# Kernel optimization log

Hardware: AMD Instinct MI355X
Metric: run time of the kernel (lower is better)

Reference implementation:

```python
import jax, jax.numpy as jnp
import numpy as np


def _gelu(x):
    return jax.nn.gelu(x, approximate=False)


def _conv2d(x, w, b, pad=0, dil=1, groups=1):
    y = jax.lax.conv_general_dilated(
        x, w, (1, 1), [(pad, pad), (pad, pad)], rhs_dilation=(dil, dil),
        dimension_numbers=('NCHW', 'OIHW', 'NCHW'), feature_group_count=groups)
    return y + b[None, :, None, None]


def _ln_last(x, g, b, eps=1e-5):
    m = jnp.mean(x, -1, keepdims=True)
    v = jnp.var(x, -1, keepdims=True)
    return (x - m) * jax.lax.rsqrt(v + eps) * g + b


def _ln2d(x, g, b, eps=1e-5):
    # LayerNorm over channel dim of NCHW
    m = jnp.mean(x, 1, keepdims=True)
    v = jnp.var(x, 1, keepdims=True)
    return (x - m) * jax.lax.rsqrt(v + eps) * g[None, :, None, None] + b[None, :, None, None]


def _bilinear(x, py, px):
    # x: [B,C,H,W]; py,px: [B,H,W] float sample coords; zero outside
    B, C, H, W = x.shape
    y0 = jnp.floor(py)
    x0 = jnp.floor(px)
    wy = py - y0
    wx = px - x0
    xf = x.reshape(B, C, H * W)

    def g(yi, xi):
        valid = ((yi >= 0) & (yi < H) & (xi >= 0) & (xi < W)).astype(x.dtype)
        yc = jnp.clip(yi, 0, H - 1).astype(jnp.int32)
        xc = jnp.clip(xi, 0, W - 1).astype(jnp.int32)
        idx = (yc * W + xc).reshape(B, 1, H * W)
        v = jnp.take_along_axis(xf, idx, axis=2).reshape(B, C, H, W)
        return v * valid[:, None]

    return (g(y0, x0) * ((1 - wy) * (1 - wx))[:, None]
            + g(y0, x0 + 1) * ((1 - wy) * wx)[:, None]
            + g(y0 + 1, x0) * (wy * (1 - wx))[:, None]
            + g(y0 + 1, x0 + 1) * (wy * wx)[:, None])


def _deform_dw(x, ow, ob, w, b, dil):
    # modulated deformable depthwise 3x3 conv, offset_groups=1
    B, C, H, W = x.shape
    pad = dil
    off = _conv2d(x, ow, ob, pad=pad, dil=dil)          # [B,27,H,W]
    ox, oy, m = jnp.split(off, 3, axis=1)               # each [B,9,H,W]
    m = jax.nn.sigmoid(m)
    ys = jnp.arange(H, dtype=x.dtype)[None, :, None]
    xs = jnp.arange(W, dtype=x.dtype)[None, None, :]
    acc = jnp.zeros_like(x)
    for ki in range(3):
        for kj in range(3):
            kk = ki * 3 + kj
            py = ys - pad + ki * dil + oy[:, kk]
            px = xs - pad + kj * dil + ox[:, kk]
            s = _bilinear(x, py, px)                    # [B,C,H,W]
            acc = acc + s * m[:, kk][:, None] * w[:, 0, ki, kj][None, :, None, None]
    return acc + b[None, :, None, None]


def _forward(image_embed, inter_prototypes, intra_prototypes, masks,
             proj_w, proj_b, lin_w, lin_b, tok_g, tok_b, alpha,
             in_w, in_b, off0_w, off0_b, dw0_w, dw0_b,
             off1_w, off1_b, dw1_w, dw1_b, cv_w, cv_b, ln_g, ln_b,
             op0_w, op0_b, op1_w, op1_b, op2_w, op2_b,
             out0_w, out0_b, out1_w, out1_b):
    C = image_embed.shape[1]
    scale = C ** -0.5
    # prototype tokens [B,Q,C]
    pt = jnp.einsum('bqc,bnc->bqn', inter_prototypes, intra_prototypes)
    t = jnp.concatenate([inter_prototypes, pt], axis=-1) @ proj_w + proj_b
    t = _gelu(t) @ lin_w + lin_b
    t = _ln_last(t, tok_g, tok_b)
    # mask gating of image features
    pe = jnp.einsum('bnc,bnhw->bchw', intra_prototypes, masks)
    img = image_embed * pe + image_embed
    # DeformAttn
    x = _gelu(_conv2d(img, in_w, in_b))
    a = _deform_dw(x, off0_w, off0_b, dw0_w, dw0_b, dil=1)
    a = _deform_dw(a, off1_w, off1_b, dw1_w, dw1_b, dil=3)
    a = _conv2d(a, cv_w, cv_b)
    x = x * a + img
    x = _ln2d(x, ln_g, ln_b)
    y = _conv2d(x, op0_w, op0_b)
    y = _gelu(_conv2d(y, op1_w, op1_b, pad=1, groups=C))
    y = _conv2d(y, op2_w, op2_b)
    dense = y + x
    # prototype cross-attention over 8 tokens
    attn = jnp.einsum('bchw,bqc->bqhw', dense, t) * scale
    attn = jax.nn.softmax(attn, axis=1)
    attn = jnp.einsum('bqhw,bqc->bchw', attn, t)
    attn = attn + dense * alpha[None, :, None, None]
    o = _gelu(_conv2d(attn, out0_w, out0_b))
    o = _conv2d(o, out1_w, out1_b)
    return o


def setup_inputs():
    key = jax.random.key(0)
    ks = jax.random.split(key, 40)
    B, C, H, W, Q, N = 16, 256, 64, 64, 8, 9
    f32 = jnp.float32

    def rn(k, shp, s=1.0):
        return jax.random.normal(k, shp, f32) * s

    inp = {
        'image_embed': rn(ks[0], (B, C, H, W)),
        'inter_prototypes': rn(ks[1], (B, Q, C)),
        'intra_prototypes': rn(ks[2], (B, N, C)),
        'masks': jax.random.uniform(ks[3], (B, N, H, W), f32),
        'proj_w': rn(ks[4], (C + N, C), 0.02), 'proj_b': jnp.zeros((C,), f32),
        'lin_w': rn(ks[5], (C, C), 0.02), 'lin_b': jnp.zeros((C,), f32),
        'tok_g': 1.0 + rn(ks[6], (C,), 0.05), 'tok_b': rn(ks[7], (C,), 0.05),
        'alpha': jnp.ones((C,), f32) * 0.001,
        'in_w': rn(ks[8], (C, C, 1, 1), 0.02), 'in_b': jnp.zeros((C,), f32),
        'off0_w': rn(ks[9], (27, C, 3, 3), 0.01), 'off0_b': rn(ks[10], (27,), 0.01),
        'dw0_w': rn(ks[11], (C, 1, 3, 3), 0.2), 'dw0_b': jnp.zeros((C,), f32),
        'off1_w': rn(ks[12], (27, C, 3, 3), 0.01), 'off1_b': rn(ks[13], (27,), 0.01),
        'dw1_w': rn(ks[14], (C, 1, 3, 3), 0.2), 'dw1_b': jnp.zeros((C,), f32),
        'cv_w': rn(ks[15], (C, C, 1, 1), 0.02), 'cv_b': jnp.zeros((C,), f32),
        'ln_g': 1.0 + rn(ks[16], (C,), 0.05), 'ln_b': rn(ks[17], (C,), 0.05),
        'op0_w': rn(ks[18], (C, C, 1, 1), 0.02), 'op0_b': jnp.zeros((C,), f32),
        'op1_w': rn(ks[19], (C, 1, 3, 3), 0.2), 'op1_b': jnp.zeros((C,), f32),
        'op2_w': rn(ks[20], (C, C, 1, 1), 0.02), 'op2_b': jnp.zeros((C,), f32),
        'out0_w': rn(ks[21], (C // 2, C, 1, 1), 0.02), 'out0_b': jnp.zeros((C // 2,), f32),
        'out1_w': rn(ks[22], (C, C // 2, 1, 1), 0.02), 'out1_b': jnp.zeros((C,), f32),
    }
    return inp


def reference(image_embed, inter_prototypes, intra_prototypes, masks,
              proj_w, proj_b, lin_w, lin_b, tok_g, tok_b, alpha,
              in_w, in_b, off0_w, off0_b, dw0_w, dw0_b,
              off1_w, off1_b, dw1_w, dw1_b, cv_w, cv_b, ln_g, ln_b,
              op0_w, op0_b, op1_w, op1_b, op2_w, op2_b,
              out0_w, out0_b, out1_w, out1_b):
    return _forward(image_embed, inter_prototypes, intra_prototypes, masks,
                    proj_w, proj_b, lin_w, lin_b, tok_g, tok_b, alpha,
                    in_w, in_b, off0_w, off0_b, dw0_w, dw0_b,
                    off1_w, off1_b, dw1_w, dw1_b, cv_w, cv_b, ln_g, ln_b,
                    op0_w, op0_b, op1_w, op1_b, op2_w, op2_b,
                    out0_w, out0_b, out1_w, out1_b)
```

## Files before the change

### kernel.cpp

```cpp
#include <hip/hip_runtime.h>
#include <math.h>

#define BB 16
#define CC 256
#define HH 64
#define WW 64
#define HWs 4096
#define PP 65536
#define QQ 8
#define NN 9

typedef _Float16 half8_t __attribute__((ext_vector_type(8)));
typedef _Float16 half4_t __attribute__((ext_vector_type(4)));
typedef _Float16 half2_t __attribute__((ext_vector_type(2)));
typedef float floatx4 __attribute__((ext_vector_type(4)));

__device__ __forceinline__ float gelu_f(float x) {
    return 0.5f * x * (1.0f + erff(x * 0.70710678118654752f));
}

__global__ void prep_weights_kernel(const float* __restrict__ off0_w, const float* __restrict__ off1_w,
                                    const float* __restrict__ dw0_w, const float* __restrict__ dw1_w,
                                    const float* __restrict__ op1_w,
                                    const float* __restrict__ in_w, const float* __restrict__ cv_w,
                                    const float* __restrict__ op0_w, const float* __restrict__ op2_w,
                                    const float* __restrict__ out0_w, const float* __restrict__ out1_w,
                                    float* __restrict__ dwt0, float* __restrict__ dwt1,
                                    float* __restrict__ op1t,
                                    _Float16* __restrict__ wh_in, _Float16* __restrict__ wh_cv,
                                    _Float16* __restrict__ wh_op0, _Float16* __restrict__ wh_op2,
                                    _Float16* __restrict__ wh_out0, _Float16* __restrict__ wh_out1,
                                    _Float16* __restrict__ whoff0, _Float16* __restrict__ whoff1) {
    int i = blockIdx.x * 256 + threadIdx.x;
    if (i < 9*256) {
        int c = i & 255;
        int tap = i >> 8;
        dwt0[i] = dw0_w[c*9 + tap];
        dwt1[i] = dw1_w[c*9 + tap];
        op1t[i] = op1_w[c*9 + tap];
    }
    if (i < 65536) {
        wh_in[i]  = (_Float16)in_w[i];
        wh_cv[i]  = (_Float16)cv_w[i];
        wh_op0[i] = (_Float16)op0_w[i];
        wh_op2[i] = (_Float16)op2_w[i];
    }
    if (i < 32768) {
        wh_out0[i] = (_Float16)out0_w[i];
        wh_out1[i] = (_Float16)out1_w[i];
    }
    if (i < 9*32*256) {
        int ci = i & 255;
        int k32 = (i >> 8) & 31;
        int tap = i >> 13;
        float v0 = 0.f, v1 = 0.f;
        if (k32 < 27) {
            v0 = off0_w[(k32*256 + ci)*9 + tap];
            v1 = off1_w[(k32*256 + ci)*9 + tap];
        }
        whoff0[i] = (_Float16)v0;
        whoff1[i] = (_Float16)v1;
    }
}

__global__ void token_kernel(const float* __restrict__ inter, const float* __restrict__ intra,
                             const float* __restrict__ proj_w, const float* __restrict__ proj_b,
                             const float* __restrict__ lin_w, const float* __restrict__ lin_b,
                             const float* __restrict__ tok_g, const float* __restrict__ tok_b,
                             float* __restrict__ t_out) {
    int bq = blockIdx.x;
    int b = bq >> 3, q = bq & 7;
    int c = threadIdx.x;
    __shared__ float inter_s[256];
    __shared__ float pt_s[9];
    __shared__ float g_s[256];
    __shared__ float red[256];
    __shared__ float stat[2];
    inter_s[c] = inter[(b*QQ + q)*CC + c];
    __syncthreads();
    for (int n = 0; n < 9; n++) {
        red[c] = inter_s[c] * intra[(b*NN + n)*CC + c];
        __syncthreads();
        for (int s = 128; s > 0; s >>= 1) {
            if (c < s) red[c] += red[c + s];
            __syncthreads();
        }
        if (c == 0) pt_s[n] = red[0];
        __syncthreads();
    }
    float u = proj_b[c];
    for (int k = 0; k < 256; k++) u += inter_s[k] * proj_w[k*CC + c];
    for (int n = 0; n < 9; n++) u += pt_s[n] * proj_w[(256 + n)*CC + c];
    g_s[c] = gelu_f(u);
    __syncthreads();
    float v = lin_b[c];
    for (int k = 0; k < 256; k++) v += g_s[k] * lin_w[k*CC + c];
    red[c] = v;
    __syncthreads();
    for (int s = 128; s > 0; s >>= 1) { if (c < s) red[c] += red[c + s]; __syncthreads(); }
    if (c == 0) stat[0] = red[0] * (1.0f/256.0f);
    __syncthreads();
    float m = stat[0];
    red[c] = (v - m)*(v - m);
    __syncthreads();
    for (int s = 128; s > 0; s >>= 1) { if (c < s) red[c] += red[c + s]; __syncthreads(); }
    if (c == 0) stat[1] = red[0] * (1.0f/256.0f);
    __syncthreads();
    float var = stat[1];
    float r = rsqrtf(var + 1e-5f);
    t_out[(b*QQ + q)*CC + c] = (v - m) * r * tok_g[c] + tok_b[c];
}

__global__ void img_pe_kernel(const float* __restrict__ ie, const float* __restrict__ intra,
                              const float* __restrict__ masks, _Float16* __restrict__ img) {
    int b = blockIdx.z;
    int c0 = blockIdx.y * 32;
    int s0 = blockIdx.x * 32;
    __shared__ float tile[32][33];
    __shared__ float intra_s[9][32];
    __shared__ float mask_s[9][32];
    int tx = threadIdx.x, ty = threadIdx.y;
    int t = ty*32 + tx;
    for (int i = t; i < 288; i += 256) {
        int n = i >> 5, j = i & 31;
        intra_s[n][j] = intra[(b*NN + n)*CC + c0 + j];
        mask_s[n][j]  = masks[(b*NN + n)*HWs + s0 + j];
    }
    __syncthreads();
    #pragma unroll
    for (int r = 0; r < 4; r++) {
        int cl = ty + 8*r;
        float val = ie[(b*CC + c0 + cl)*HWs + s0 + tx];
        float pe = 0.f;
        #pragma unroll
        for (int n = 0; n < 9; n++) pe += intra_s[n][cl] * mask_s[n][tx];
        tile[cl][tx] = val * (1.0f + pe);
    }
    __syncthreads();
    #pragma unroll
    for (int r = 0; r < 4; r++) {
        int sl = ty + 8*r;
        img[(b*HWs + s0 + sl)*CC + c0 + tx] = (_Float16)tile[tx][sl];
    }
}

template<int CI, int CO, int ACT, int RES, int OUT>
__global__ void __launch_bounds__(256) conv1x1_mfma(const _Float16* __restrict__ in, const _Float16* __restrict__ Wh,
        const float* __restrict__ bias, const _Float16* __restrict__ res, float* __restrict__ out,
        _Float16* __restrict__ outh) {
    constexpr int KS = CI/32;
    constexpr int NF = CO/64;
    constexpr int LDR = CI + 8;
    __shared__ __align__(16) _Float16 a_lds[64*LDR];
    int t = threadIdx.x;
    int wid = t >> 6, lane = t & 63;
    int quad = lane >> 4, l16 = lane & 15;
    int p0 = blockIdx.x * 64;
    {
        const half8_t* inh = (const half8_t*)in + (size_t)p0*(CI/8);
        for (int i = t; i < 64*(CI/8); i += 256) {
            int r = i/(CI/8), c8 = i%(CI/8);
            *(half8_t*)&a_lds[r*LDR + c8*8] = inh[i];
        }
    }
    __syncthreads();
    int n0 = wid*(CO/4);
    floatx4 acc[4][NF];
    #pragma unroll
    for (int mf = 0; mf < 4; mf++)
        #pragma unroll
        for (int nf = 0; nf < NF; nf++)
            #pragma unroll
            for (int r = 0; r < 4; r++) acc[mf][nf][r] = 0.f;
    for (int ks = 0; ks < KS; ks++) {
        int k = ks*32 + quad*8;
        half8_t a[4];
        #pragma unroll
        for (int mf = 0; mf < 4; mf++)
            a[mf] = *(const half8_t*)&a_lds[(mf*16 + l16)*LDR + k];
        half8_t bfr[NF];
        #pragma unroll
        for (int nf = 0; nf < NF; nf++) {
            int brow = (OUT == 1) ? (n0 + l16*NF + nf) : (n0 + nf*16 + l16);
            bfr[nf] = *(const half8_t*)&Wh[(size_t)brow*CI + k];
        }
        #pragma unroll
        for (int mf = 0; mf < 4; mf++)
            #pragma unroll
            for (int nf = 0; nf < NF; nf++)
                acc[mf][nf] = __builtin_amdgcn_mfma_f32_16x16x32_f16(a[mf], bfr[nf], acc[mf][nf], 0, 0, 0);
    }
    if (OUT == 1) {
        int cb = n0 + l16*NF;
        float bs[NF];
        #pragma unroll
        for (int j = 0; j < NF; j++) bs[j] = bias[cb + j];
        #pragma unroll
        for (int mf = 0; mf < 4; mf++) {
            #pragma unroll
            for (int r = 0; r < 4; r++) {
                int p = p0 + mf*16 + quad*4 + r;
                half4_t rh;
                if (RES == 2 && NF == 4) rh = *(const half4_t*)&res[(size_t)p*CO + cb];
                _Float16 tmp[NF];
                #pragma unroll
                for (int j = 0; j < NF; j++) {
                    float v = acc[mf][j][r] + bs[j];
                    if (ACT) v = gelu_f(v);
                    if (RES == 2 && NF == 4) v += (float)rh[j];
                    tmp[j] = (_Float16)v;
                }
                if (NF == 4) {
                    half4_t o4; o4[0]=tmp[0]; o4[1]=tmp[1]; o4[2]=tmp[2]; o4[3]=tmp[3];
                    *(half4_t*)&outh[(size_t)p*CO + cb] = o4;
                } else {
                    half2_t o2; o2[0]=tmp[0]; o2[1]=tmp[1];
                    *(half2_t*)&outh[(size_t)p*CO + cb] = o2;
                }
            }
        }
    } else {
        size_t bb = (size_t)(p0 >> 12) * ((size_t)CO * HWs) + (size_t)(p0 & 4095);
        #pragma unroll
        for (int nf = 0; nf < NF; nf++) {
            int co = n0 + nf*16 + l16;
            float bs = bias[co];
            #pragma unroll
            for (int mf = 0; mf < 4; mf++) {
                float4 vst;
                vst.x = acc[mf][nf][0] + bs;
                vst.y = acc[mf][nf][1] + bs;
                vst.z = acc[mf][nf][2] + bs;
                vst.w = acc[mf][nf][3] + bs;
                if (ACT) { vst.x=gelu_f(vst.x); vst.y=gelu_f(vst.y); vst.z=gelu_f(vst.z); vst.w=gelu_f(vst.w); }
                *(float4*)&out[bb + (size_t)co*HWs + mf*16 + quad*4] = vst;
            }
        }
    }
}

__global__ void __launch_bounds__(256) conv_cv_ln_kernel(const _Float16* __restrict__ in, const _Float16* __restrict__ Wh,
        const float* __restrict__ bias, const _Float16* __restrict__ X, const _Float16* __restrict__ IMG,
        const float* __restrict__ g, const float* __restrict__ bb2, _Float16* __restrict__ out) {
    constexpr int CI = 256, KS = 8, NF = 4, LDR = 264;
    __shared__ __align__(16) _Float16 a_lds[64*LDR];
    __shared__ float rs[64][4];
    __shared__ float rs2[64][4];
    __shared__ float st[64][2];
    int t = threadIdx.x;
    int wid = t >> 6, lane = t & 63;
    int quad = lane >> 4, l16 = lane & 15;
    int p0 = blockIdx.x * 64;
    {
        const half8_t* inh = (const half8_t*)in + (size_t)p0*32;
        for (int i = t; i < 2048; i += 256) {
            int r = i >> 5, c8 = i & 31;
            *(half8_t*)&a_lds[r*LDR + c8*8] = inh[i];
        }
    }
    __syncthreads();
    int n0 = wid*64;
    floatx4 acc[4][4];
    #pragma unroll
    for (int mf = 0; mf < 4; mf++)
        #pragma unroll
        for (int nf = 0; nf < 4; nf++)
            #pragma unroll
            for (int r = 0; r < 4; r++) acc[mf][nf][r] = 0.f;
    for (int ks = 0; ks < KS; ks++) {
        int k = ks*32 + quad*8;
        half8_t a[4];
        #pragma unroll
        for (int mf = 0; mf < 4; mf++)
            a[mf] = *(const half8_t*)&a_lds[(mf*16 + l16)*LDR + k];
        half8_t bfr[4];
        #pragma unroll
        for (int nf = 0; nf < 4; nf++)
            bfr[nf] = *(const half8_t*)&Wh[(size_t)(n0 + l16*4 + nf)*CI + k];
        #pragma unroll
        for (int mf = 0; mf < 4; mf++)
            #pragma unroll
            for (int nf = 0; nf < 4; nf++)
                acc[mf][nf] = __builtin_amdgcn_mfma_f32_16x16x32_f16(a[mf], bfr[nf], acc[mf][nf], 0, 0, 0);
    }
    int cb = n0 + l16*4;
    float bs[4];
    #pragma unroll
    for (int j = 0; j < 4; j++) bs[j] = bias[cb + j];
    #pragma unroll
    for (int mf = 0; mf < 4; mf++) {
        #pragma unroll
        for (int r = 0; r < 4; r++) {
            int px_l = mf*16 + quad*4 + r;
            size_t off = (size_t)(p0 + px_l)*256 + cb;
            half4_t xh = *(const half4_t*)&X[off];
            half4_t ih = *(const half4_t*)&IMG[off];
            float s = 0.f, s2 = 0.f;
            #pragma unroll
            for (int j = 0; j < 4; j++) {
                float v = acc[mf][j][r] + bs[j];
                v = (float)xh[j]*v + (float)ih[j];
                acc[mf][j][r] = v;
                s += v; s2 += v*v;
            }
            s += __shfl_xor(s, 1); s2 += __shfl_xor(s2, 1);
            s += __shfl_xor(s, 2); s2 += __shfl_xor(s2, 2);
            s += __shfl_xor(s, 4); s2 += __shfl_xor(s2, 4);
            s += __shfl_xor(s, 8); s2 += __shfl_xor(s2, 8);
            if (l16 == 0) { rs[px_l][wid] = s; rs2[px_l][wid] = s2; }
        }
    }
    __syncthreads();
    if (t < 64) {
        float m = 0.f, q = 0.f;
        #pragma unroll
        for (int w = 0; w < 4; w++) { m += rs[t][w]; q += rs2[t][w]; }
        m *= (1.0f/256.0f);
        float var = q*(1.0f/256.0f) - m*m;
        st[t][0] = m;
        st[t][1] = rsqrtf(var + 1e-5f);
    }
    __syncthreads();
    float ga[4], ba[4];
    #pragma unroll
    for (int j = 0; j < 4; j++) { ga[j] = g[cb + j]; ba[j] = bb2[cb + j]; }
    #pragma unroll
    for (int mf = 0; mf < 4; mf++) {
        #pragma unroll
        for (int r = 0; r < 4; r++) {
            int px_l = mf*16 + quad*4 + r;
            float m = st[px_l][0];
            float ri = st[px_l][1];
            half4_t o4;
            #pragma unroll
            for (int j = 0; j < 4; j++)
                o4[j] = (_Float16)((acc[mf][j][r] - m)*ri*ga[j] + ba[j]);
            *(half4_t*)&out[(size_t)(p0 + px_l)*256 + cb] = o4;
        }
    }
}

template<int DIL>
__global__ void __launch_bounds__(256) off_conv_mfma(const _Float16* __restrict__ x, const _Float16* __restrict__ Wh,
        const float* __restrict__ bias, float* __restrict__ off) {
    constexpr int LDR = 264;
    __shared__ __align__(16) _Float16 xs[70*LDR];
    int raw = blockIdx.x;
    int bh = (raw & 7) * 128 + (raw >> 3);
    int b = bh >> 6, h = bh & 63;
    int t = threadIdx.x;
    int wid = t >> 6, lane = t & 63;
    int quad = lane >> 4, l16 = lane & 15;
    for (int i = t; i < 6*LDR; i += 256) {
        int r = i/LDR, c = i%LDR;
        int row = (r < 3) ? r : (64 + r);
        xs[row*LDR + c] = (_Float16)0.f;
    }
    floatx4 acc[2];
    #pragma unroll
    for (int nf = 0; nf < 2; nf++)
        #pragma unroll
        for (int r = 0; r < 4; r++) acc[nf][r] = 0.f;
    for (int ki = 0; ki < 3; ki++) {
        int hrow = h + (ki - 1)*DIL;
        __syncthreads();
        if (hrow >= 0 && hrow < 64) {
            const half8_t* row = (const half8_t*)(x + ((size_t)(b*64 + hrow)*64) * 256);
            for (int i = t; i < 2048; i += 256) {
                int r = i >> 5, c8 = i & 31;
                *(half8_t*)&xs[(r + 3)*LDR + c8*8] = row[r*32 + c8];
            }
        } else {
            half8_t z = (half8_t)((_Float16)0.f);
            for (int i = t; i < 2048; i += 256) {
                int r = i >> 5, c8 = i & 31;
                *(half8_t*)&xs[(r + 3)*LDR + c8*8] = z;
            }
        }
        __syncthreads();
        #pragma unroll
        for (int kj = 0; kj < 3; kj++) {
            const _Float16* wt = Wh + (size_t)(ki*3 + kj)*32*256;
            int wrow = wid*16 + l16 + (kj - 1)*DIL + 3;
            #pragma unroll
            for (int cs = 0; cs < 8; cs++) {
                int k = cs*32 + quad*8;
                half8_t a = *(const half8_t*)&xs[wrow*LDR + k];
                half8_t b0 = *(const half8_t*)&wt[(size_t)l16*256 + k];
                half8_t b1 = *(const half8_t*)&wt[(size_t)(16 + l16)*256 + k];
                acc[0] = __builtin_amdgcn_mfma_f32_16x16x32_f16(a, b0, acc[0], 0, 0, 0);
                acc[1] = __builtin_amdgcn_mfma_f32_16x16x32_f16(a, b1, acc[1], 0, 0, 0);
            }
        }
    }
    int pbase = (b*64 + h)*64;
    #pragma unroll
    for (int nf = 0; nf < 2; nf++) {
        int kcol = nf*16 + l16;
        if (kcol < 27) {
            float bs = bias[kcol];
            #pragma unroll
            for (int r = 0; r < 4; r++) {
                int w = wid*16 + quad*4 + r;
                off[(size_t)(pbase + w)*27 + kcol] = acc[nf][r] + bs;
            }
        }
    }
}

template<int DIL>
__global__ void __launch_bounds__(256) deform_kernel(const _Float16* __restrict__ src, const float* __restrict__ off,
        const float* __restrict__ dwt, const float* __restrict__ dwb, _Float16* __restrict__ out) {
    int raw = blockIdx.x;
    int swz = (raw & 7) * 256 + (raw >> 3);
    int whalf = swz & 1;
    int bh = swz >> 1;
    int b = bh >> 6, h = bh & 63;
    int t = threadIdx.x;
    int c4 = t & 63;
    int ps = t >> 6;

    __shared__ float4 wq4[288];
    __shared__ int4   iq4[288];
    __shared__ float  dw_lds[9*256];

    for (int i = t; i < 9*256; i += 256) dw_lds[i] = dwt[i];

    for (int j = t; j < 288; j += 256) {
        int lw = j / 9;
        int kk = j - lw*9;
        int w = whalf*32 + lw;
        int p = (b*64 + h)*64 + w;
        const float* op = off + (size_t)p*27;
        float ox = op[kk];
        float oy = op[9 + kk];
        float mm = op[18 + kk];
        mm = 1.0f / (1.0f + expf(-mm));
        int ki = kk / 3, kj = kk - ki*3;
        float py = (float)(h - DIL + ki*DIL) + oy;
        float px = (float)(w - DIL + kj*DIL) + ox;
        float y0f = floorf(py), x0f = floorf(px);
        float wy = py - y0f, wx = px - x0f;
        int y0 = (int)y0f, x0 = (int)x0f;
        int y1 = y0 + 1, x1 = x0 + 1;
        float w00 = (1.f - wy)*(1.f - wx)*mm;
        float w01 = (1.f - wy)*wx*mm;
        float w10 = wy*(1.f - wx)*mm;
        float w11 = wy*wx*mm;
        bool yv0 = (y0 >= 0) && (y0 < 64);
        bool yv1 = (y1 >= 0) && (y1 < 64);
        bool xv0 = (x0 >= 0) && (x0 < 64);
        bool xv1 = (x1 >= 0) && (x1 < 64);
        int y0c = min(max(y0, 0), 63), y1c = min(max(y1, 0), 63);
        int x0c = min(max(x0, 0), 63), x1c = min(max(x1, 0), 63);
        int base = b*4096;
        float4 wv;
        wv.x = (yv0 && xv0) ? w00 : 0.f;
        wv.y = (yv0 && xv1) ? w01 : 0.f;
        wv.z = (yv1 && xv0) ? w10 : 0.f;
        wv.w = (yv1 && xv1) ? w11 : 0.f;
        wq4[j] = wv;
        int4 iv;
        iv.x = (base + y0c*64 + x0c) << 9;
        iv.y = (base + y0c*64 + x1c) << 9;
        iv.z = (base + y1c*64 + x0c) << 9;
        iv.w = (base + y1c*64 + x1c) << 9;
        iq4[j] = iv;
    }
    __syncthreads();

    float4 bv = ((const float4*)dwb)[c4];
    const char* srcb = (const char*)src + (size_t)c4*8;
    for (int i = 0; i < 8; i++) {
        int lw = ps*8 + i;
        int jb = lw*9;
        int w = whalf*32 + lw;
        int p = (b*64 + h)*64 + w;
        half4_t v[9][4];
        #pragma unroll
        for (int kk = 0; kk < 9; kk++) {
            int4 iv = iq4[jb + kk];
            int o0 = __builtin_amdgcn_readfirstlane(iv.x);
            int o1 = __builtin_amdgcn_readfirstlane(iv.y);
            int o2 = __builtin_amdgcn_readfirstlane(iv.z);
            int o3 = __builtin_amdgcn_readfirstlane(iv.w);
            v[kk][0] = *(const half4_t*)(srcb + o0);
            v[kk][1] = *(const half4_t*)(srcb + o1);
            v[kk][2] = *(const half4_t*)(srcb + o2);
            v[kk][3] = *(const half4_t*)(srcb + o3);
        }
        __builtin_amdgcn_sched_barrier(0);
        float4 acc = make_float4(0.f,0.f,0.f,0.f);
        #pragma unroll
        for (int kk = 0; kk < 9; kk++) {
            float4 wv = wq4[jb + kk];
            float4 dw = ((const float4*)dw_lds)[kk*64 + c4];
            float sx = (float)v[kk][0][0]*wv.x + (float)v[kk][1][0]*wv.y + (float)v[kk][2][0]*wv.z + (float)v[kk][3][0]*wv.w;
            float sy = (float)v[kk][0][1]*wv.x + (float)v[kk][1][1]*wv.y + (float)v[kk][2][1]*wv.z + (float)v[kk][3][1]*wv.w;
            float sz = (float)v[kk][0][2]*wv.x + (float)v[kk][1][2]*wv.y + (float)v[kk][2][2]*wv.z + (float)v[kk][3][2]*wv.w;
            float sw = (float)v[kk][0][3]*wv.x + (float)v[kk][1][3]*wv.y + (float)v[kk][2][3]*wv.z + (float)v[kk][3][3]*wv.w;
            acc.x += sx * dw.x;
            acc.y += sy * dw.y;
            acc.z += sz * dw.z;
            acc.w += sw * dw.w;
        }
        half4_t o4;
        o4[0] = (_Float16)(acc.x + bv.x);
        o4[1] = (_Float16)(acc.y + bv.y);
        o4[2] = (_Float16)(acc.z + bv.z);
        o4[3] = (_Float16)(acc.w + bv.w);
        ((half4_t*)out)[(size_t)p*64 + c4] = o4;
    }
}

__global__ void __launch_bounds__(256) dw3x3_kernel(const _Float16* __restrict__ in, const float* __restrict__ wt,
        const float* __restrict__ bias, _Float16* __restrict__ out) {
    int raw = blockIdx.x;
    int swz = (raw & 7) * 2048 + (raw >> 3);
    int gid = swz*256 + threadIdx.x;
    int c4 = gid & 63;
    int p = gid >> 6;
    int w = p & 63;
    int h = (p >> 6) & 63;
    int b = p >> 12;
    float4 acc = ((const float4*)bias)[c4];
    #pragma unroll
    for (int ki = 0; ki < 3; ki++) {
        int hh = h + ki - 1;
        if (hh < 0 || hh >= 64) continue;
        #pragma unroll
        for (int kj = 0; kj < 3; kj++) {
            int wwp = w + kj - 1;
            if (wwp < 0 || wwp >= 64) continue;
            half4_t v = ((const half4_t*)in)[((b*64 + hh)*64 + wwp)*64 + c4];
            float4 wv = ((const float4*)wt)[(ki*3 + kj)*64 + c4];
            acc.x += (float)v[0]*wv.x; acc.y += (float)v[1]*wv.y;
            acc.z += (float)v[2]*wv.z; acc.w += (float)v[3]*wv.w;
        }
    }
    half4_t o4;
    o4[0] = (_Float16)gelu_f(acc.x);
    o4[1] = (_Float16)gelu_f(acc.y);
    o4[2] = (_Float16)gelu_f(acc.z);
    o4[3] = (_Float16)gelu_f(acc.w);
    ((half4_t*)out)[p*64 + c4] = o4;
}

__global__ void __launch_bounds__(256) attn_mfma_kernel(const _Float16* __restrict__ dense,
        const float* __restrict__ tok, const float* __restrict__ alpha, _Float16* __restrict__ out) {
    __shared__ __align__(16) _Float16 d_lds[64*264];
    __shared__ __align__(16) _Float16 t_q[16*264];
    __shared__ __align__(16) _Float16 t_t[258*24];
    __shared__ __align__(16) _Float16 w_lds[64*40];
    __shared__ float al_s[256];
    int t = threadIdx.x;
    int wid = t >> 6, lane = t & 63;
    int quad = lane >> 4, l16 = lane & 15;
    int p0 = blockIdx.x * 64;
    int b = p0 >> 12;

    for (int i = t; i < 16*264; i += 256) t_q[i] = (_Float16)0.f;
    for (int i = t; i < 258*24; i += 256) t_t[i] = (_Float16)0.f;
    for (int i = t; i < 64*40;  i += 256) w_lds[i] = (_Float16)0.f;
    __syncthreads();

    const half8_t* dh = (const half8_t*)dense + (size_t)p0*32;
    for (int i = t; i < 2048; i += 256) {
        int r = i >> 5, c8 = i & 31;
        *(half8_t*)&d_lds[r*264 + c8*8] = dh[i];
    }
    for (int i = t; i < 512; i += 256) {
        int q = i >> 6, j = i & 63;
        float4 tv = ((const float4*)tok)[(b*8 + q)*64 + j];
        int c0 = j*4;
        t_q[q*264 + c0 + 0] = (_Float16)tv.x;
        t_q[q*264 + c0 + 1] = (_Float16)tv.y;
        t_q[q*264 + c0 + 2] = (_Float16)tv.z;
        t_q[q*264 + c0 + 3] = (_Float16)tv.w;
        t_t[(c0 + 0)*24 + q] = (_Float16)tv.x;
        t_t[(c0 + 1)*24 + q] = (_Float16)tv.y;
        t_t[(c0 + 2)*24 + q] = (_Float16)tv.z;
        t_t[(c0 + 3)*24 + q] = (_Float16)tv.w;
    }
    al_s[t] = alpha[t];
    __syncthreads();

    floatx4 s4;
    s4[0]=0.f; s4[1]=0.f; s4[2]=0.f; s4[3]=0.f;
    #pragma unroll
    for (int ks = 0; ks < 8; ks++) {
        int k = ks*32 + quad*8;
        half8_t a = *(const half8_t*)&d_lds[(wid*16 + l16)*264 + k];
        half8_t bf = *(const half8_t*)&t_q[l16*264 + k];
        s4 = __builtin_amdgcn_mfma_f32_16x16x32_f16(a, bf, s4, 0, 0, 0);
    }
    float wgt[4];
    #pragma unroll
    for (int r = 0; r < 4; r++) {
        float sc = s4[r] * 0.0625f;
        float mx = sc;
        mx = fmaxf(mx, __shfl_xor(mx, 1));
        mx = fmaxf(mx, __shfl_xor(mx, 2));
        mx = fmaxf(mx, __shfl_xor(mx, 4));
        float e = expf(sc - mx);
        float dn = e;
        dn += __shfl_xor(dn, 1);
        dn += __shfl_xor(dn, 2);
        dn += __shfl_xor(dn, 4);
        wgt[r] = e / dn;
    }
    if (l16 < 8) {
        #pragma unroll
        for (int r = 0; r < 4; r++)
            w_lds[(wid*16 + quad*4 + r)*40 + l16] = (_Float16)wgt[r];
    }
    __syncthreads();

    half8_t aw = *(const half8_t*)&w_lds[(wid*16 + l16)*40 + quad*8];
    floatx4 z4; z4[0]=0.f; z4[1]=0.f; z4[2]=0.f; z4[3]=0.f;
    floatx4 acc[16];
    #pragma unroll
    for (int nf = 0; nf < 16; nf++) {
        half8_t bf = *(const half8_t*)&t_t[(nf*16 + l16)*24 + quad*8];
        acc[nf] = __builtin_amdgcn_mfma_f32_16x16x32_f16(aw, bf, z4, 0, 0, 0);
    }
    #pragma unroll
    for (int nf = 0; nf < 16; nf++) {
        int co = nf*16 + l16;
        float al = al_s[co];
        #pragma unroll
        for (int r = 0; r < 4; r++) {
            int px = wid*16 + quad*4 + r;
            float d = (float)d_lds[px*264 + co];
            float o = acc[nf][r] + d*al;
            out[(size_t)(p0 + px)*256 + co] = (_Float16)o;
        }
    }
}

extern "C" void kernel_launch(void* const* d_in, const int* in_sizes, int n_in,
                              void* d_out, int out_size, void* d_ws, size_t ws_size,
                              hipStream_t stream) {
    const float* image_embed = (const float*)d_in[0];
    const float* inter_p     = (const float*)d_in[1];
    const float* intra_p     = (const float*)d_in[2];
    const float* masks       = (const float*)d_in[3];
    const float* proj_w      = (const float*)d_in[4];
    const float* proj_b      = (const float*)d_in[5];
    const float* lin_w       = (const float*)d_in[6];
    const float* lin_b       = (const float*)d_in[7];
    const float* tok_g       = (const float*)d_in[8];
    const float* tok_b       = (const float*)d_in[9];
    const float* alpha       = (const float*)d_in[10];
    const float* in_w        = (const float*)d_in[11];
    const float* in_b        = (const float*)d_in[12];
    const float* off0_w      = (const float*)d_in[13];
    const float* off0_b      = (const float*)d_in[14];
    const float* dw0_w       = (const float*)d_in[15];
    const float* dw0_b       = (const float*)d_in[16];
    const float* off1_w      = (const float*)d_in[17];
    const float* off1_b      = (const float*)d_in[18];
    const float* dw1_w       = (const float*)d_in[19];
    const float* dw1_b       = (const float*)d_in[20];
    const float* cv_w        = (const float*)d_in[21];
    const float* cv_b        = (const float*)d_in[22];
    const float* ln_g        = (const float*)d_in[23];
    const float* ln_b        = (const float*)d_in[24];
    const float* op0_w       = (const float*)d_in[25];
    const float* op0_b       = (const float*)d_in[26];
    const float* op1_w       = (const float*)d_in[27];
    const float* op1_b       = (const float*)d_in[28];
    const float* op2_w       = (const float*)d_in[29];
    const float* op2_b       = (const float*)d_in[30];
    const float* out0_w      = (const float*)d_in[31];
    const float* out0_b      = (const float*)d_in[32];
    const float* out1_w      = (const float*)d_in[33];
    const float* out1_b      = (const float*)d_in[34];
    (void)ws_size; (void)in_sizes; (void)n_in; (void)out_size;

    float* ws = (float*)d_ws;
    const size_t BIG = (size_t)PP * CC;
    float* A   = ws;
    float* Bb  = A + BIG;
    float* Cb  = Bb + BIG;
    float* OFF = Cb + BIG;
    float* TOK = OFF + (size_t)PP*27;
    float* DWT0 = TOK + BB*QQ*CC;
    float* DWT1 = DWT0 + 9*256;
    float* OP1T = DWT1 + 9*256;
    _Float16* WH_IN   = (_Float16*)(OP1T + 9*256);
    _Float16* WH_CV   = WH_IN + 65536;
    _Float16* WH_OP0  = WH_CV + 65536;
    _Float16* WH_OP2  = WH_OP0 + 65536;
    _Float16* WH_OUT0 = WH_OP2 + 65536;
    _Float16* WH_OUT1 = WH_OUT0 + 32768;
    _Float16* WHOFF0  = WH_OUT1 + 32768;
    _Float16* WHOFF1  = WHOFF0 + 9*32*256;
    _Float16* IMGH = (_Float16*)A;
    _Float16* Y0H  = (_Float16*)A;
    _Float16* Y1H  = Y0H + (size_t)PP*CC;
    _Float16* XH   = (_Float16*)Bb;
    _Float16* A1H  = XH + (size_t)PP*CC;
    _Float16* ATH  = (_Float16*)Bb;
    _Float16* A2H  = (_Float16*)Cb;
    _Float16* DENH = (_Float16*)Cb;
    _Float16* O0H  = (_Float16*)Cb + (size_t)PP*CC;
    _Float16* XLNH = (_Float16*)d_out;

    prep_weights_kernel<<<(9*32*256 + 255)/256, 256, 0, stream>>>(
        off0_w, off1_w, dw0_w, dw1_w, op1_w,
        in_w, cv_w, op0_w, op2_w, out0_w, out1_w,
        DWT0, DWT1, OP1T,
        WH_IN, WH_CV, WH_OP0, WH_OP2, WH_OUT0, WH_OUT1, WHOFF0, WHOFF1);
    token_kernel<<<BB*QQ, 256, 0, stream>>>(inter_p, intra_p, proj_w, proj_b,
                                            lin_w, lin_b, tok_g, tok_b, TOK);
    img_pe_kernel<<<dim3(HWs/32, CC/32, BB), dim3(32,8), 0, stream>>>(image_embed, intra_p, masks, IMGH);
    conv1x1_mfma<256,256,1,0,1><<<PP/64, 256, 0, stream>>>(IMGH, WH_IN, in_b, nullptr, nullptr, XH);
    off_conv_mfma<1><<<BB*HH, 256, 0, stream>>>(XH, WHOFF0, off0_b, OFF);
    deform_kernel<1><<<BB*HH*2, 256, 0, stream>>>(XH, OFF, DWT0, dw0_b, A1H);
    off_conv_mfma<3><<<BB*HH, 256, 0, stream>>>(A1H, WHOFF1, off1_b, OFF);
    deform_kernel<3><<<BB*HH*2, 256, 0, stream>>>(A1H, OFF, DWT1, dw1_b, A2H);
    conv_cv_ln_kernel<<<PP/64, 256, 0, stream>>>(A2H, WH_CV, cv_b, XH, IMGH, ln_g, ln_b, XLNH);
    conv1x1_mfma<256,256,0,0,1><<<PP/64, 256, 0, stream>>>(XLNH, WH_OP0, op0_b, nullptr, nullptr, Y0H);
    dw3x3_kernel<<<PP*64/256, 256, 0, stream>>>(Y0H, OP1T, op1_b, Y1H);
    conv1x1_mfma<256,256,0,2,1><<<PP/64, 256, 0, stream>>>(Y1H, WH_OP2, op2_b, XLNH, nullptr, DENH);
    attn_mfma_kernel<<<PP/64, 256, 0, stream>>>(DENH, TOK, alpha, ATH);
    conv1x1_mfma<256,128,1,0,1><<<PP/64, 256, 0, stream>>>(ATH, WH_OUT0, out0_b, nullptr, nullptr, O0H);
    conv1x1_mfma<128,256,0,0,3><<<PP/64, 256, 0, stream>>>(O0H, WH_OUT1, out1_b, nullptr, (float*)d_out, nullptr);
}
```

Baseline: 769.9 us.

## Fuse attention with both output 1x1 convs and split deform rows into quarters

The attention kernel now keeps its result in shared memory and runs the out0 (GELU) and out1 1x1 convolutions in the same block, writing the final NCHW float output directly. This removes two kernel launches and two full-size fp16 intermediate round-trips through global memory. The deform kernels now give each block a quarter row (16 pixels) instead of a half row, doubling the grid to raise occupancy, at the cost of recomputing per-block setup such as the depthwise weight load. The conv1x1 template loses its NCHW float output path, and the fused kernel uses more shared memory, which may lower its occupancy.

Measured after the change: 776.9 us. No clear change (+0.9%).

```diff
diff --git a/kernel.cpp b/kernel.cpp
--- a/kernel.cpp
+++ b/kernel.cpp
@@ -181,7 +181,7 @@
         half8_t bfr[NF];
         #pragma unroll
         for (int nf = 0; nf < NF; nf++) {
-            int brow = (OUT == 1) ? (n0 + l16*NF + nf) : (n0 + nf*16 + l16);
+            int brow = n0 + l16*NF + nf;
             bfr[nf] = *(const half8_t*)&Wh[(size_t)brow*CI + k];
         }
         #pragma unroll
@@ -190,50 +190,31 @@
             for (int nf = 0; nf < NF; nf++)
                 acc[mf][nf] = __builtin_amdgcn_mfma_f32_16x16x32_f16(a[mf], bfr[nf], acc[mf][nf], 0, 0, 0);
     }
-    if (OUT == 1) {
-        int cb = n0 + l16*NF;
-        float bs[NF];
-        #pragma unroll
-        for (int j = 0; j < NF; j++) bs[j] = bias[cb + j];
-        #pragma unroll
-        for (int mf = 0; mf < 4; mf++) {
-            #pragma unroll
-            for (int r = 0; r < 4; r++) {
-                int p = p0 + mf*16 + quad*4 + r;
-                half4_t rh;
-                if (RES == 2 && NF == 4) rh = *(const half4_t*)&res[(size_t)p*CO + cb];
-                _Float16 tmp[NF];
-                #pragma unroll
-                for (int j = 0; j < NF; j++) {
-                    float v = acc[mf][j][r] + bs[j];
-                    if (ACT) v = gelu_f(v);
-                    if (RES == 2 && NF == 4) v += (float)rh[j];
-                    tmp[j] = (_Float16)v;
-                }
-                if (NF == 4) {
-                    half4_t o4; o4[0]=tmp[0]; o4[1]=tmp[1]; o4[2]=tmp[2]; o4[3]=tmp[3];
-                    *(half4_t*)&outh[(size_t)p*CO + cb] = o4;
-                } else {
-                    half2_t o2; o2[0]=tmp[0]; o2[1]=tmp[1];
-                    *(half2_t*)&outh[(size_t)p*CO + cb] = o2;
-                }
+    int cb = n0 + l16*NF;
+    float bs[NF];
+    #pragma unroll
+    for (int j = 0; j < NF; j++) bs[j] = bias[cb + j];
+    #pragma unroll
+    for (int mf = 0; mf < 4; mf++) {
+        #pragma unroll
+        for (int r = 0; r < 4; r++) {
+            int p = p0 + mf*16 + quad*4 + r;
+            half4_t rh;
+            if (RES == 2 && NF == 4) rh = *(const half4_t*)&res[(size_t)p*CO + cb];
+            _Float16 tmp[NF];
+            #pragma unroll
+            for (int j = 0; j < NF; j++) {
+                float v = acc[mf][j][r] + bs[j];
+                if (ACT) v = gelu_f(v);
+                if (RES == 2 && NF == 4) v += (float)rh[j];
+                tmp[j] = (_Float16)v;
             }
-        }
-    } else {
-        size_t bb = (size_t)(p0 >> 12) * ((size_t)CO * HWs) + (size_t)(p0 & 4095);
-        #pragma unroll
-        for (int nf = 0; nf < NF; nf++) {
-            int co = n0 + nf*16 + l16;
-            float bs = bias[co];
-            #pragma unroll
-            for (int mf = 0; mf < 4; mf++) {
-                float4 vst;
-                vst.x = acc[mf][nf][0] + bs;
-                vst.y = acc[mf][nf][1] + bs;
-                vst.z = acc[mf][nf][2] + bs;
-                vst.w = acc[mf][nf][3] + bs;
-                if (ACT) { vst.x=gelu_f(vst.x); vst.y=gelu_f(vst.y); vst.z=gelu_f(vst.z); vst.w=gelu_f(vst.w); }
-                *(float4*)&out[bb + (size_t)co*HWs + mf*16 + quad*4] = vst;
+            if (NF == 4) {
+                half4_t o4; o4[0]=tmp[0]; o4[1]=tmp[1]; o4[2]=tmp[2]; o4[3]=tmp[3];
+                *(half4_t*)&outh[(size_t)p*CO + cb] = o4;
+            } else {
+                half2_t o2; o2[0]=tmp[0]; o2[1]=tmp[1];
+                *(half2_t*)&outh[(size_t)p*CO + cb] = o2;
             }
         }
     }
@@ -242,7 +223,7 @@
 __global__ void __launch_bounds__(256) conv_cv_ln_kernel(const _Float16* __restrict__ in, const _Float16* __restrict__ Wh,
         const float* __restrict__ bias, const _Float16* __restrict__ X, const _Float16* __restrict__ IMG,
         const float* __restrict__ g, const float* __restrict__ bb2, _Float16* __restrict__ out) {
-    constexpr int CI = 256, KS = 8, NF = 4, LDR = 264;
+    constexpr int CI = 256, KS = 8, LDR = 264;
     __shared__ __align__(16) _Float16 a_lds[64*LDR];
     __shared__ float rs[64][4];
     __shared__ float rs2[64][4];
@@ -412,24 +393,24 @@
 __global__ void __launch_bounds__(256) deform_kernel(const _Float16* __restrict__ src, const float* __restrict__ off,
         const float* __restrict__ dwt, const float* __restrict__ dwb, _Float16* __restrict__ out) {
     int raw = blockIdx.x;
-    int swz = (raw & 7) * 256 + (raw >> 3);
-    int whalf = swz & 1;
-    int bh = swz >> 1;
+    int swz = (raw & 7) * 512 + (raw >> 3);
+    int wq = swz & 3;
+    int bh = swz >> 2;
     int b = bh >> 6, h = bh & 63;
     int t = threadIdx.x;
     int c4 = t & 63;
     int ps = t >> 6;
 
-    __shared__ float4 wq4[288];
-    __shared__ int4   iq4[288];
+    __shared__ float4 wq4[144];
+    __shared__ int4   iq4[144];
     __shared__ float  dw_lds[9*256];
 
     for (int i = t; i < 9*256; i += 256) dw_lds[i] = dwt[i];
 
-    for (int j = t; j < 288; j += 256) {
+    for (int j = t; j < 144; j += 256) {
         int lw = j / 9;
         int kk = j - lw*9;
-        int w = whalf*32 + lw;
+        int w = wq*16 + lw;
         int p = (b*64 + h)*64 + w;
         const float* op = off + (size_t)p*27;
         float ox = op[kk];
@@ -471,10 +452,10 @@
 
     float4 bv = ((const float4*)dwb)[c4];
     const char* srcb = (const char*)src + (size_t)c4*8;
-    for (int i = 0; i < 8; i++) {
-        int lw = ps*8 + i;
+    for (int i = 0; i < 4; i++) {
+        int lw = ps*4 + i;
         int jb = lw*9;
-        int w = whalf*32 + lw;
+        int w = wq*16 + lw;
         int p = (b*64 + h)*64 + w;
         half4_t v[9][4];
         #pragma unroll
@@ -546,12 +527,16 @@
     ((half4_t*)out)[p*64 + c4] = o4;
 }
 
-__global__ void __launch_bounds__(256) attn_mfma_kernel(const _Float16* __restrict__ dense,
-        const float* __restrict__ tok, const float* __restrict__ alpha, _Float16* __restrict__ out) {
-    __shared__ __align__(16) _Float16 d_lds[64*264];
+__global__ void __launch_bounds__(256) attn_out_fused(const _Float16* __restrict__ dense,
+        const float* __restrict__ tok, const float* __restrict__ alpha,
+        const _Float16* __restrict__ W0, const float* __restrict__ b0,
+        const _Float16* __restrict__ W1, const float* __restrict__ b1,
+        float* __restrict__ out) {
+    __shared__ __align__(16) _Float16 d_att[64*264];
     __shared__ __align__(16) _Float16 t_q[16*264];
-    __shared__ __align__(16) _Float16 t_t[258*24];
+    __shared__ __align__(16) _Float16 t_t[256*32];
     __shared__ __align__(16) _Float16 w_lds[64*40];
+    __shared__ __align__(16) _Float16 o0_lds[64*136];
     __shared__ float al_s[256];
     int t = threadIdx.x;
     int wid = t >> 6, lane = t & 63;
@@ -560,14 +545,14 @@
     int b = p0 >> 12;
 
     for (int i = t; i < 16*264; i += 256) t_q[i] = (_Float16)0.f;
-    for (int i = t; i < 258*24; i += 256) t_t[i] = (_Float16)0.f;
+    for (int i = t; i < 256*32; i += 256) t_t[i] = (_Float16)0.f;
     for (int i = t; i < 64*40;  i += 256) w_lds[i] = (_Float16)0.f;
     __syncthreads();
 
     const half8_t* dh = (const half8_t*)dense + (size_t)p0*32;
     for (int i = t; i < 2048; i += 256) {
         int r = i >> 5, c8 = i & 31;
-        *(half8_t*)&d_lds[r*264 + c8*8] = dh[i];
+        *(half8_t*)&d_att[r*264 + c8*8] = dh[i];
     }
     for (int i = t; i < 512; i += 256) {
         int q = i >> 6, j = i & 63;
@@ -577,10 +562,10 @@
         t_q[q*264 + c0 + 1] = (_Float16)tv.y;
         t_q[q*264 + c0 + 2] = (_Float16)tv.z;
         t_q[q*264 + c0 + 3] = (_Float16)tv.w;
-        t_t[(c0 + 0)*24 + q] = (_Float16)tv.x;
-        t_t[(c0 + 1)*24 + q] = (_Float16)tv.y;
-        t_t[(c0 + 2)*24 + q] = (_Float16)tv.z;
-        t_t[(c0 + 3)*24 + q] = (_Float16)tv.w;
+        t_t[(c0 + 0)*32 + q] = (_Float16)tv.x;
+        t_t[(c0 + 1)*32 + q] = (_Float16)tv.y;
+        t_t[(c0 + 2)*32 + q] = (_Float16)tv.z;
+        t_t[(c0 + 3)*32 + q] = (_Float16)tv.w;
     }
     al_s[t] = alpha[t];
     __syncthreads();
@@ -590,7 +575,7 @@
     #pragma unroll
     for (int ks = 0; ks < 8; ks++) {
         int k = ks*32 + quad*8;
-        half8_t a = *(const half8_t*)&d_lds[(wid*16 + l16)*264 + k];
+        half8_t a = *(const half8_t*)&d_att[(wid*16 + l16)*264 + k];
         half8_t bf = *(const half8_t*)&t_q[l16*264 + k];
         s4 = __builtin_amdgcn_mfma_f32_16x16x32_f16(a, bf, s4, 0, 0, 0);
     }
@@ -618,22 +603,110 @@
 
     half8_t aw = *(const half8_t*)&w_lds[(wid*16 + l16)*40 + quad*8];
     floatx4 z4; z4[0]=0.f; z4[1]=0.f; z4[2]=0.f; z4[3]=0.f;
-    floatx4 acc[16];
+    floatx4 acc2[16];
     #pragma unroll
     for (int nf = 0; nf < 16; nf++) {
-        half8_t bf = *(const half8_t*)&t_t[(nf*16 + l16)*24 + quad*8];
-        acc[nf] = __builtin_amdgcn_mfma_f32_16x16x32_f16(aw, bf, z4, 0, 0, 0);
-    }
-    #pragma unroll
-    for (int nf = 0; nf < 16; nf++) {
-        int co = nf*16 + l16;
-        float al = al_s[co];
+        half8_t bf = *(const half8_t*)&t_t[(l16*16 + nf)*32 + quad*8];
+        acc2[nf] = __builtin_amdgcn_mfma_f32_16x16x32_f16(aw, bf, z4, 0, 0, 0);
+    }
+    int cb = l16*16;
+    float alv[16];
+    #pragma unroll
+    for (int nf = 0; nf < 16; nf++) alv[nf] = al_s[cb + nf];
+    #pragma unroll
+    for (int r = 0; r < 4; r++) {
+        int px = wid*16 + quad*4 + r;
+        half8_t dlo = *(const half8_t*)&d_att[px*264 + cb];
+        half8_t dhi = *(const half8_t*)&d_att[px*264 + cb + 8];
+        half8_t olo, ohi;
+        #pragma unroll
+        for (int nf = 0; nf < 8; nf++) {
+            olo[nf] = (_Float16)(acc2[nf][r]     + (float)dlo[nf]*alv[nf]);
+            ohi[nf] = (_Float16)(acc2[nf + 8][r] + (float)dhi[nf]*alv[nf + 8]);
+        }
+        *(half8_t*)&d_att[px*264 + cb] = olo;
+        *(half8_t*)&d_att[px*264 + cb + 8] = ohi;
+    }
+    __syncthreads();
+
+    int n0 = wid*32;
+    floatx4 acc0[4][2];
+    #pragma unroll
+    for (int mf = 0; mf < 4; mf++)
+        #pragma unroll
+        for (int nf = 0; nf < 2; nf++)
+            #pragma unroll
+            for (int r = 0; r < 4; r++) acc0[mf][nf][r] = 0.f;
+    #pragma unroll
+    for (int ks = 0; ks < 8; ks++) {
+        int k = ks*32 + quad*8;
+        half8_t a[4];
+        #pragma unroll
+        for (int mf = 0; mf < 4; mf++)
+            a[mf] = *(const half8_t*)&d_att[(mf*16 + l16)*264 + k];
+        half8_t bf[2];
+        #pragma unroll
+        for (int nf = 0; nf < 2; nf++)
+            bf[nf] = *(const half8_t*)&W0[(size_t)(n0 + l16*2 + nf)*256 + k];
+        #pragma unroll
+        for (int mf = 0; mf < 4; mf++)
+            #pragma unroll
+            for (int nf = 0; nf < 2; nf++)
+                acc0[mf][nf] = __builtin_amdgcn_mfma_f32_16x16x32_f16(a[mf], bf[nf], acc0[mf][nf], 0, 0, 0);
+    }
+    int cb0 = n0 + l16*2;
+    float bs0[2] = { b0[cb0], b0[cb0 + 1] };
+    #pragma unroll
+    for (int mf = 0; mf < 4; mf++) {
         #pragma unroll
         for (int r = 0; r < 4; r++) {
-            int px = wid*16 + quad*4 + r;
-            float d = (float)d_lds[px*264 + co];
-            float o = acc[nf][r] + d*al;
-            out[(size_t)(p0 + px)*256 + co] = (_Float16)o;
+            int px = mf*16 + quad*4 + r;
+            half2_t o2;
+            o2[0] = (_Float16)gelu_f(acc0[mf][0][r] + bs0[0]);
+            o2[1] = (_Float16)gelu_f(acc0[mf][1][r] + bs0[1]);
+            *(half2_t*)&o0_lds[px*136 + cb0] = o2;
+        }
+    }
+    __syncthreads();
+
+    int n1 = wid*64;
+    floatx4 acc1[4][4];
+    #pragma unroll
+    for (int mf = 0; mf < 4; mf++)
+        #pragma unroll
+        for (int nf = 0; nf < 4; nf++)
+            #pragma unroll
+            for (int r = 0; r < 4; r++) acc1[mf][nf][r] = 0.f;
+    #pragma unroll
+    for (int ks = 0; ks < 4; ks++) {
+        int k = ks*32 + quad*8;
+        half8_t a[4];
+        #pragma unroll
+        for (int mf = 0; mf < 4; mf++)
+            a[mf] = *(const half8_t*)&o0_lds[(mf*16 + l16)*136 + k];
+        half8_t bf[4];
+        #pragma unroll
+        for (int nf = 0; nf < 4; nf++)
+            bf[nf] = *(const half8_t*)&W1[(size_t)(n1 + nf*16 + l16)*128 + k];
+        #pragma unroll
+        for (int mf = 0; mf < 4; mf++)
+            #pragma unroll
+            for (int nf = 0; nf < 4; nf++)
+                acc1[mf][nf] = __builtin_amdgcn_mfma_f32_16x16x32_f16(a[mf], bf[nf], acc1[mf][nf], 0, 0, 0);
+    }
+    size_t bb = (size_t)b * ((size_t)CC * HWs) + (size_t)(p0 & 4095);
+    #pragma unroll
+    for (int nf = 0; nf < 4; nf++) {
+        int co = n1 + nf*16 + l16;
+        float bs = b1[co];
+        #pragma unroll
+        for (int mf = 0; mf < 4; mf++) {
+            float4 vst;
+            vst.x = acc1[mf][nf][0] + bs;
+            vst.y = acc1[mf][nf][1] + bs;
+            vst.z = acc1[mf][nf][2] + bs;
+            vst.w = acc1[mf][nf][3] + bs;
+            *(float4*)&out[bb + (size_t)co*HWs + mf*16 + quad*4] = vst;
         }
     }
 }
@@ -701,10 +774,8 @@
     _Float16* Y1H  = Y0H + (size_t)PP*CC;
     _Float16* XH   = (_Float16*)Bb;
     _Float16* A1H  = XH + (size_t)PP*CC;
-    _Float16* ATH  = (_Float16*)Bb;
     _Float16* A2H  = (_Float16*)Cb;
     _Float16* DENH = (_Float16*)Cb;
-    _Float16* O0H  = (_Float16*)Cb + (size_t)PP*CC;
     _Float16* XLNH = (_Float16*)d_out;
 
     prep_weights_kernel<<<(9*32*256 + 255)/256, 256, 0, stream>>>(
@@ -717,14 +788,13 @@
     img_pe_kernel<<<dim3(HWs/32, CC/32, BB), dim3(32,8), 0, stream>>>(image_embed, intra_p, masks, IMGH);
     conv1x1_mfma<256,256,1,0,1><<<PP/64, 256, 0, stream>>>(IMGH, WH_IN, in_b, nullptr, nullptr, XH);
     off_conv_mfma<1><<<BB*HH, 256, 0, stream>>>(XH, WHOFF0, off0_b, OFF);
-    deform_kernel<1><<<BB*HH*2, 256, 0, stream>>>(XH, OFF, DWT0, dw0_b, A1H);
+    deform_kernel<1><<<BB*HH*4, 256, 0, stream>>>(XH, OFF, DWT0, dw0_b, A1H);
     off_conv_mfma<3><<<BB*HH, 256, 0, stream>>>(A1H, WHOFF1, off1_b, OFF);
-    deform_kernel<3><<<BB*HH*2, 256, 0, stream>>>(A1H, OFF, DWT1, dw1_b, A2H);
+    deform_kernel<3><<<BB*HH*4, 256, 0, stream>>>(A1H, OFF, DWT1, dw1_b, A2H);
     conv_cv_ln_kernel<<<PP/64, 256, 0, stream>>>(A2H, WH_CV, cv_b, XH, IMGH, ln_g, ln_b, XLNH);
     conv1x1_mfma<256,256,0,0,1><<<PP/64, 256, 0, stream>>>(XLNH, WH_OP0, op0_b, nullptr, nullptr, Y0H);
     dw3x3_kernel<<<PP*64/256, 256, 0, stream>>>(Y0H, OP1T, op1_b, Y1H);
     conv1x1_mfma<256,256,0,2,1><<<PP/64, 256, 0, stream>>>(Y1H, WH_OP2, op2_b, XLNH, nullptr, DENH);
-    attn_mfma_kernel<<<PP/64, 256, 0, stream>>>(DENH, TOK, alpha, ATH);
-    conv1x1_mfma<256,128,1,0,1><<<PP/64, 256, 0, stream>>>(ATH, WH_OUT0, out0_b, nullptr, nullptr, O0H);
-    conv1x1_mfma<128,256,0,0,3><<<PP/64, 256, 0, stream>>>(O0H, WH_OUT1, out1_b, nullptr, (float*)d_out, nullptr);
-}
+    attn_out_fused<<<PP/64, 256, 0, stream>>>(DENH, TOK, alpha,
+                                              WH_OUT0, out0_b, WH_OUT1, out1_b, (float*)d_out);
+}
```
